# Optimization experiments

Hardware: AMD Instinct MI355X
Metric: run time of the kernel (lower is better)

The kernel has to match this reference:

```python
import jax, jax.numpy as jnp
import numpy as np

HIDDEN = 256
B, SQ, SKV = 8, 2048, 2048
SCALE = float(np.sqrt(HIDDEN / 2.0))  # module uses sqrt(hidden_dim/2)


def setup_inputs() -> dict:
    key = jax.random.key(0)
    ks = jax.random.split(key, 9)
    s = 1.0 / np.sqrt(HIDDEN)
    return {
        "query": jax.random.normal(ks[0], (B, SQ, HIDDEN), jnp.float32),
        "key": jax.random.normal(ks[1], (B, SKV, HIDDEN), jnp.float32),
        "value": jax.random.normal(ks[2], (B, SKV, HIDDEN), jnp.float32),
        "Wq": jax.random.uniform(ks[3], (HIDDEN, HIDDEN), jnp.float32, -s, s),
        "bq": jax.random.uniform(ks[4], (HIDDEN,), jnp.float32, -s, s),
        "Wk": jax.random.uniform(ks[5], (HIDDEN, HIDDEN), jnp.float32, -s, s),
        "bk": jax.random.uniform(ks[6], (HIDDEN,), jnp.float32, -s, s),
        "Wv": jax.random.uniform(ks[7], (HIDDEN, HIDDEN), jnp.float32, -s, s),
        "bv": jax.random.uniform(ks[8], (HIDDEN,), jnp.float32, -s, s),
    }


def reference(query, key, value, Wq, bq, Wk, bk, Wv, bv):
    # Linear projections (torch Linear: x @ W.T + b)
    Q = jnp.einsum('bsd,ed->bse', query, Wq) + bq  # [B,SQ,H]
    K = jnp.einsum('bsd,ed->bse', key, Wk) + bk    # [B,SKV,H]
    V = jnp.einsum('bsd,ed->bse', value, Wv) + bv  # [B,SKV,H]
    scores = jnp.einsum('bqd,bkd->bqk', Q, K) / SCALE  # [B,SQ,SKV]
    weights = jax.nn.softmax(scores, axis=-1)
    return jnp.einsum('bqk,bkd->bqd', weights, V)  # [B,SQ,H]
```

## Files before the change

kernel.cpp:

```cpp
#include <hip/hip_runtime.h>

#define HID 256
#define NB 8
#define SQL 2048
#define SKV 2048
#define SPLIT 4
#define KPB (SKV / SPLIT)
#define KVB 32
#define NT (KPB / KVB)
#define NROW (NB * SQL)

typedef __attribute__((ext_vector_type(8))) short bf16x8;
typedef __attribute__((ext_vector_type(4))) float f32x4;
typedef __attribute__((ext_vector_type(16))) float f32x16;

static __device__ __forceinline__ unsigned short f2bf(float x) {
  union { float f; unsigned int u; } v; v.f = x;
  unsigned int r = v.u + 0x7FFFu + ((v.u >> 16) & 1u);
  return (unsigned short)(r >> 16);
}

__global__ void wconv_kernel(const float* __restrict__ Wq, const float* __restrict__ Wk,
                             const float* __restrict__ Wv, unsigned short* __restrict__ out) {
  int i = blockIdx.x * blockDim.x + threadIdx.x;
  if (i >= 3 * HID * HID) return;
  const float* src = (i < HID * HID) ? Wq : (i < 2 * HID * HID ? Wk : Wv);
  out[i] = f2bf(src[i & (HID * HID - 1)]);
}

__global__ __launch_bounds__(512, 4) void proj_kernel(
    const float* __restrict__ query, const float* __restrict__ key, const float* __restrict__ value,
    const unsigned short* __restrict__ Wb,
    const float* __restrict__ bq, const float* __restrict__ bk, const float* __restrict__ bv,
    unsigned short* __restrict__ Qb, unsigned short* __restrict__ Kb, unsigned short* __restrict__ Vtb) {
  __shared__ __align__(16) char wl[65536];
  int tid = threadIdx.x;
  int wave = tid >> 6, lane = tid & 63, lr = lane & 15, lg = lane >> 4;
  int blk = blockIdx.x;
  int mat = blk >> 8;
  int rem = blk & 255;
  int b = rem >> 5;
  int rt = (rem >> 1) & 15;
  int et = rem & 1;

  const float* X = (mat == 0) ? query : (mat == 1 ? key : value);
  const float* bias = (mat == 0) ? bq : (mat == 1 ? bk : bv);
  const char* Wsrc = (const char*)(Wb + mat * HID * HID + et * 128 * HID);

#pragma unroll
  for (int i = 0; i < 8; i++) {
    int c = i * 512 + tid;
    int e = c >> 5;
    int glo = e * 512 + (((c & 31) ^ (e & 7)) << 4);
    __builtin_amdgcn_global_load_lds(
        (const __attribute__((address_space(1))) unsigned int*)(Wsrc + glo),
        (__attribute__((address_space(3))) unsigned int*)(wl + c * 16), 16, 0, 0);
  }

  int row_a = rt * 128 + wave * 16 + lr;
  const float* xrow = X + ((size_t)(b * SQL + row_a)) * HID;
  bf16x8 af[8];
#pragma unroll
  for (int s = 0; s < 8; s++) {
    const float4* p = (const float4*)(xrow + s * 32 + lg * 8);
    float4 x0 = p[0], x1 = p[1];
    bf16x8 a;
    a[0] = (short)f2bf(x0.x); a[1] = (short)f2bf(x0.y); a[2] = (short)f2bf(x0.z); a[3] = (short)f2bf(x0.w);
    a[4] = (short)f2bf(x1.x); a[5] = (short)f2bf(x1.y); a[6] = (short)f2bf(x1.z); a[7] = (short)f2bf(x1.w);
    af[s] = a;
  }
  __syncthreads();

  int row_c = rt * 128 + wave * 16 + lg * 4;
#pragma unroll
  for (int eo = 0; eo < 8; eo++) {
    f32x4 acc = (f32x4){0.f, 0.f, 0.f, 0.f};
    int eL = eo * 16 + lr;
#pragma unroll
    for (int sl = 0; sl < 8; sl++) {
      bf16x8 bfr = *(const bf16x8*)(wl + eL * 512 + (((sl * 4 + lg) ^ (eL & 7)) << 4));
      acc = __builtin_amdgcn_mfma_f32_16x16x32_bf16(af[sl], bfr, acc, 0, 0, 0);
    }
    int e = et * 128 + eo * 16 + lr;
    float bv_ = bias[e];
    if (mat < 2) {
      unsigned short* dst = (mat == 0 ? Qb : Kb) + (size_t)(b * SQL) * HID;
#pragma unroll
      for (int i = 0; i < 4; i++)
        dst[(size_t)(row_c + i) * HID + e] = f2bf(acc[i] + bv_);
    } else {
      ushort4 v;
      v.x = f2bf(acc[0] + bv_); v.y = f2bf(acc[1] + bv_);
      v.z = f2bf(acc[2] + bv_); v.w = f2bf(acc[3] + bv_);
      *(ushort4*)(Vtb + ((size_t)(b * HID + e)) * SKV + row_c) = v;
    }
  }
}

__global__ __launch_bounds__(256, 2) void attn_kernel(
    const unsigned short* __restrict__ Qb, const unsigned short* __restrict__ Kb,
    const unsigned short* __restrict__ Vtb, unsigned short* __restrict__ Op,
    float* __restrict__ Ml) {
  __shared__ __align__(16) char KA[16384];
  __shared__ __align__(16) char KB[16384];
  __shared__ __align__(16) char VA[16384];
  __shared__ __align__(16) char VB[16384];
  int tid = threadIdx.x;
  int wave = tid >> 6, lane = tid & 63, l31 = lane & 31, h = lane >> 5;
  int bid = (blockIdx.x & 7) * 64 + (blockIdx.x >> 3);
  int b = bid >> 6, s = (bid >> 4) & 3, qt = bid & 15;
  int qrow0 = qt * 128 + wave * 32;
  int k0 = s * KPB;

  const char* Kc0 = (const char*)(Kb + (size_t)b * SKV * HID) + (size_t)k0 * (HID * 2);
  const char* Vc0 = (const char*)(Vtb + (size_t)b * HID * SKV) + (size_t)k0 * 2;

  int offK[4], offV[4];
#pragma unroll
  for (int i = 0; i < 4; i++) {
    int g = i * 256 + tid;
    int ky = g >> 5, cs = g & 31;
    offK[i] = ky * 512 + ((cs ^ ky) << 4);
    int d = g >> 2, ccs = g & 3;
    int cc = ccs ^ ((d >> 3) & 3);
    offV[i] = d * (SKV * 2) + cc * 16;
  }

  auto stage = [&](int t, char* kdst, char* vdst) {
    const char* Ksrc = Kc0 + t * (KVB * HID * 2);
    const char* Vsrc = Vc0 + t * (KVB * 2);
#pragma unroll
    for (int i = 0; i < 4; i++)
      __builtin_amdgcn_global_load_lds(
          (const __attribute__((address_space(1))) unsigned int*)(Ksrc + offK[i]),
          (__attribute__((address_space(3))) unsigned int*)(kdst + (i * 256 + tid) * 16),
          16, 0, 0);
#pragma unroll
    for (int i = 0; i < 4; i++)
      __builtin_amdgcn_global_load_lds(
          (const __attribute__((address_space(1))) unsigned int*)(Vsrc + offV[i]),
          (__attribute__((address_space(3))) unsigned int*)(vdst + (i * 256 + tid) * 16),
          16, 0, 0);
  };

  bf16x8 qf[16];
  {
    const unsigned short* qrow = Qb + ((size_t)(b * SQL + qrow0 + l31)) * HID + h * 8;
#pragma unroll
    for (int ks = 0; ks < 16; ks++) qf[ks] = *(const bf16x8*)(qrow + ks * 16);
  }

  f32x16 acc[8];
#pragma unroll
  for (int dt = 0; dt < 8; dt++)
#pragma unroll
    for (int j = 0; j < 16; j++) acc[dt][j] = 0.f;

  float m = -1e30f, l = 0.f;
  const float kC = 1.44269504088896341f / 11.3137084989847604f;

  auto step = [&](const char* kb, const char* vb) {
    f32x16 p, p1;
#pragma unroll
    for (int j = 0; j < 16; j++) { p[j] = 0.f; p1[j] = 0.f; }
#pragma unroll
    for (int ks = 0; ks < 8; ks++) {
      bf16x8 kf0 = *(const bf16x8*)(kb + l31 * 512 + (((ks * 2 + h) ^ l31) << 4));
      bf16x8 kf1 = *(const bf16x8*)(kb + l31 * 512 + ((((ks + 8) * 2 + h) ^ l31) << 4));
      p = __builtin_amdgcn_mfma_f32_32x32x16_bf16(kf0, qf[ks], p, 0, 0, 0);
      p1 = __builtin_amdgcn_mfma_f32_32x32x16_bf16(kf1, qf[ks + 8], p1, 0, 0, 0);
    }
#pragma unroll
    for (int j = 0; j < 16; j++) p[j] += p1[j];

    float tmax = p[0];
#pragma unroll
    for (int j = 1; j < 16; j++) tmax = fmaxf(tmax, p[j]);
    tmax = fmaxf(tmax, __shfl_xor(tmax, 32, 64));
    float msc = tmax * kC;
    if (!__all(msc <= m + 8.0f)) {
      float mn = fmaxf(m, msc);
      float al = exp2f(m - mn);
      l *= al;
      m = mn;
#pragma unroll
      for (int r = 0; r < 16; r++) {
        int qp = (r & 3) + 8 * (r >> 2) + 4 * h;
        float ar = __shfl(al, qp, 64);
#pragma unroll
        for (int dt = 0; dt < 8; dt++) acc[dt][r] *= ar;
      }
    }
#pragma unroll
    for (int j = 0; j < 16; j++) p[j] = exp2f(fmaf(p[j], kC, -m));
    float ts = 0.f;
#pragma unroll
    for (int j = 0; j < 16; j++) ts += p[j];
    ts += __shfl_xor(ts, 32, 64);
    l += ts;

#pragma unroll
    for (int k2 = 0; k2 < 2; k2++) {
      unsigned P0, P1, P2, P3;
      asm("v_cvt_pk_bf16_f32 %0, %1, %2" : "=v"(P0) : "v"(p[k2 * 8 + 0]), "v"(p[k2 * 8 + 1]));
      asm("v_cvt_pk_bf16_f32 %0, %1, %2" : "=v"(P1) : "v"(p[k2 * 8 + 2]), "v"(p[k2 * 8 + 3]));
      asm("v_cvt_pk_bf16_f32 %0, %1, %2" : "=v"(P2) : "v"(p[k2 * 8 + 4]), "v"(p[k2 * 8 + 5]));
      asm("v_cvt_pk_bf16_f32 %0, %1, %2" : "=v"(P3) : "v"(p[k2 * 8 + 6]), "v"(p[k2 * 8 + 7]));
      asm("v_permlane32_swap_b32 %0, %1" : "+v"(P0), "+v"(P2));
      asm("v_permlane32_swap_b32 %0, %1" : "+v"(P1), "+v"(P3));
      union { unsigned u[4]; bf16x8 v; } pa;
      pa.u[0] = P0; pa.u[1] = P1; pa.u[2] = P2; pa.u[3] = P3;
      int ccs_base = k2 * 2 + h;
#pragma unroll
      for (int dt = 0; dt < 8; dt++) {
        int ccs = (ccs_base ^ ((l31 >> 3) & 3)) & 3;
        bf16x8 vf = *(const bf16x8*)(vb + dt * 2048 + l31 * 64 + ccs * 16);
        acc[dt] = __builtin_amdgcn_mfma_f32_32x32x16_bf16(pa.v, vf, acc[dt], 0, 0, 0);
      }
    }
  };

  stage(0, KA, VA);
  __syncthreads();
  for (int t = 0; t < NT; t++) {
    char* kb = (t & 1) ? KB : KA;
    char* vb = (t & 1) ? VB : VA;
    if (t + 1 < NT) stage(t + 1, (t & 1) ? KA : KB, (t & 1) ? VA : VB);
    step(kb, vb);
    __syncthreads();
  }

  if (h == 0) {
    size_t row = (size_t)b * SQL + qrow0 + l31;
    float2 ml; ml.x = m; ml.y = l;
    *(float2*)(Ml + ((size_t)s * NROW + row) * 2) = ml;
  }
#pragma unroll
  for (int r = 0; r < 16; r++) {
    int qp = (r & 3) + 8 * (r >> 2) + 4 * h;
    float linv = 1.0f / __shfl(l, qp, 64);
    size_t row = (size_t)b * SQL + qrow0 + qp;
#pragma unroll
    for (int dt = 0; dt < 8; dt++) {
      union { _Float16 hf; unsigned short u; } cv;
      cv.hf = (_Float16)(acc[dt][r] * linv);
      Op[((size_t)s * NROW + row) * HID + dt * 32 + l31] = cv.u;
    }
  }
}

__global__ __launch_bounds__(256) void comb_kernel(const unsigned short* __restrict__ Op,
                                                   const float* __restrict__ Ml,
                                                   float* __restrict__ out) {
  int idx = blockIdx.x * 256 + threadIdx.x;
  int row = idx >> 6;
  int d0 = (idx & 63) << 2;
  float mv[SPLIT], lv[SPLIT];
#pragma unroll
  for (int s = 0; s < SPLIT; s++) {
    float2 ml = *(const float2*)(Ml + ((size_t)s * NROW + row) * 2);
    mv[s] = ml.x; lv[s] = ml.y;
  }
  float M = mv[0];
#pragma unroll
  for (int s = 1; s < SPLIT; s++) M = fmaxf(M, mv[s]);
  float W = 0.f, w[SPLIT];
#pragma unroll
  for (int s = 0; s < SPLIT; s++) { w[s] = lv[s] * exp2f(mv[s] - M); W += w[s]; }
  float wi = 1.0f / W;
  float o0 = 0.f, o1 = 0.f, o2 = 0.f, o3 = 0.f;
#pragma unroll
  for (int s = 0; s < SPLIT; s++) {
    ushort4 u = *(const ushort4*)(Op + ((size_t)s * NROW + row) * HID + d0);
    union { unsigned short us; _Float16 hf; } c0, c1, c2, c3;
    c0.us = u.x; c1.us = u.y; c2.us = u.z; c3.us = u.w;
    o0 += w[s] * (float)c0.hf; o1 += w[s] * (float)c1.hf;
    o2 += w[s] * (float)c2.hf; o3 += w[s] * (float)c3.hf;
  }
  float4 res; res.x = o0 * wi; res.y = o1 * wi; res.z = o2 * wi; res.w = o3 * wi;
  *(float4*)(out + (size_t)row * HID + d0) = res;
}

extern "C" void kernel_launch(void* const* d_in, const int* in_sizes, int n_in,
                              void* d_out, int out_size, void* d_ws, size_t ws_size,
                              hipStream_t stream) {
  const float* query = (const float*)d_in[0];
  const float* key   = (const float*)d_in[1];
  const float* value = (const float*)d_in[2];
  const float* Wq = (const float*)d_in[3];
  const float* bq = (const float*)d_in[4];
  const float* Wk = (const float*)d_in[5];
  const float* bk = (const float*)d_in[6];
  const float* Wv = (const float*)d_in[7];
  const float* bv = (const float*)d_in[8];

  char* ws = (char*)d_ws;
  unsigned short* Wb  = (unsigned short*)ws;
  unsigned short* Qb  = (unsigned short*)(ws + 393216);
  unsigned short* Kb  = Qb + (size_t)NB * SQL * HID;
  unsigned short* Vtb = Kb + (size_t)NB * SKV * HID;
  unsigned short* Op  = Vtb + (size_t)NB * HID * SKV;
  float* Ml = (float*)(Op + (size_t)SPLIT * NROW * HID);

  hipLaunchKernelGGL(wconv_kernel, dim3(768), dim3(256), 0, stream, Wq, Wk, Wv, Wb);
  hipLaunchKernelGGL(proj_kernel, dim3(768), dim3(512), 0, stream,
                     query, key, value, Wb, bq, bk, bv, Qb, Kb, Vtb);
  hipLaunchKernelGGL(attn_kernel, dim3(512), dim3(256), 0, stream, Qb, Kb, Vtb, Op, Ml);
  hipLaunchKernelGGL(comb_kernel, dim3(4096), dim3(256), 0, stream, Op, Ml, (float*)d_out);
}
```

Measured before the change: 108.0 us.

## Rewrite attention to 16x16 MFMA tiles with direct global K/V loads

Reworks the attention kernel so each wave handles 16 query rows using 16x16x32 bf16 MFMAs instead of 32x32x16. K and V fragments are loaded straight from global memory into registers, replacing the double-buffered LDS staging; only a small per-wave LDS buffer remains to transpose P. The KV split drops from 4 to 2, which halves the partial outputs the combine kernel must merge. The cost is more redundant global/L2 traffic for K/V, since waves no longer share staged tiles, and less overlap between loads and compute.

```diff
diff --git a/kernel.cpp b/kernel.cpp
--- a/kernel.cpp
+++ b/kernel.cpp
@@ -4,7 +4,7 @@
 #define NB 8
 #define SQL 2048
 #define SKV 2048
-#define SPLIT 4
+#define SPLIT 2
 #define KPB (SKV / SPLIT)
 #define KVB 32
 #define NT (KPB / KVB)
@@ -12,7 +12,6 @@
 
 typedef __attribute__((ext_vector_type(8))) short bf16x8;
 typedef __attribute__((ext_vector_type(4))) float f32x4;
-typedef __attribute__((ext_vector_type(16))) float f32x16;
 
 static __device__ __forceinline__ unsigned short f2bf(float x) {
   union { float f; unsigned int u; } v; v.f = x;
@@ -101,150 +100,112 @@
     const unsigned short* __restrict__ Qb, const unsigned short* __restrict__ Kb,
     const unsigned short* __restrict__ Vtb, unsigned short* __restrict__ Op,
     float* __restrict__ Ml) {
-  __shared__ __align__(16) char KA[16384];
-  __shared__ __align__(16) char KB[16384];
-  __shared__ __align__(16) char VA[16384];
-  __shared__ __align__(16) char VB[16384];
+  __shared__ __align__(16) char PB[4][1024];
   int tid = threadIdx.x;
-  int wave = tid >> 6, lane = tid & 63, l31 = lane & 31, h = lane >> 5;
-  int bid = (blockIdx.x & 7) * 64 + (blockIdx.x >> 3);
-  int b = bid >> 6, s = (bid >> 4) & 3, qt = bid & 15;
-  int qrow0 = qt * 128 + wave * 32;
-  int k0 = s * KPB;
-
-  const char* Kc0 = (const char*)(Kb + (size_t)b * SKV * HID) + (size_t)k0 * (HID * 2);
-  const char* Vc0 = (const char*)(Vtb + (size_t)b * HID * SKV) + (size_t)k0 * 2;
-
-  int offK[4], offV[4];
-#pragma unroll
-  for (int i = 0; i < 4; i++) {
-    int g = i * 256 + tid;
-    int ky = g >> 5, cs = g & 31;
-    offK[i] = ky * 512 + ((cs ^ ky) << 4);
-    int d = g >> 2, ccs = g & 3;
-    int cc = ccs ^ ((d >> 3) & 3);
-    offV[i] = d * (SKV * 2) + cc * 16;
-  }
-
-  auto stage = [&](int t, char* kdst, char* vdst) {
-    const char* Ksrc = Kc0 + t * (KVB * HID * 2);
-    const char* Vsrc = Vc0 + t * (KVB * 2);
-#pragma unroll
-    for (int i = 0; i < 4; i++)
-      __builtin_amdgcn_global_load_lds(
-          (const __attribute__((address_space(1))) unsigned int*)(Ksrc + offK[i]),
-          (__attribute__((address_space(3))) unsigned int*)(kdst + (i * 256 + tid) * 16),
-          16, 0, 0);
-#pragma unroll
-    for (int i = 0; i < 4; i++)
-      __builtin_amdgcn_global_load_lds(
-          (const __attribute__((address_space(1))) unsigned int*)(Vsrc + offV[i]),
-          (__attribute__((address_space(3))) unsigned int*)(vdst + (i * 256 + tid) * 16),
-          16, 0, 0);
-  };
-
-  bf16x8 qf[16];
+  int wave = tid >> 6, lane = tid & 63, l15 = lane & 15, g = lane >> 4;
+  int j = blockIdx.x;
+  int p_ = (j & 7) + ((j >> 8) & 1) * 8;
+  int i_ = (j >> 3) & 31;
+  int b = p_ >> 1, s = p_ & 1;
+  int q0 = (i_ * 4 + wave) * 16;
+
+  const unsigned short* Kbase = Kb + ((size_t)b * SKV + (size_t)s * KPB) * HID;
+  const unsigned short* Vbase = Vtb + (size_t)b * HID * SKV + (size_t)s * KPB;
+
+  bf16x8 qf[8];
   {
-    const unsigned short* qrow = Qb + ((size_t)(b * SQL + qrow0 + l31)) * HID + h * 8;
-#pragma unroll
-    for (int ks = 0; ks < 16; ks++) qf[ks] = *(const bf16x8*)(qrow + ks * 16);
-  }
-
-  f32x16 acc[8];
-#pragma unroll
-  for (int dt = 0; dt < 8; dt++)
-#pragma unroll
-    for (int j = 0; j < 16; j++) acc[dt][j] = 0.f;
-
-  float m = -1e30f, l = 0.f;
+    const unsigned short* qrow = Qb + ((size_t)(b * SQL + q0 + l15)) * HID + g * 8;
+#pragma unroll
+    for (int sl = 0; sl < 8; sl++) qf[sl] = *(const bf16x8*)(qrow + sl * 32);
+  }
+
+  f32x4 acc[16];
+#pragma unroll
+  for (int dt = 0; dt < 16; dt++) acc[dt] = (f32x4){0.f, 0.f, 0.f, 0.f};
+  float m = -1e30f, lsum = 0.f;
   const float kC = 1.44269504088896341f / 11.3137084989847604f;
-
-  auto step = [&](const char* kb, const char* vb) {
-    f32x16 p, p1;
-#pragma unroll
-    for (int j = 0; j < 16; j++) { p[j] = 0.f; p1[j] = 0.f; }
-#pragma unroll
-    for (int ks = 0; ks < 8; ks++) {
-      bf16x8 kf0 = *(const bf16x8*)(kb + l31 * 512 + (((ks * 2 + h) ^ l31) << 4));
-      bf16x8 kf1 = *(const bf16x8*)(kb + l31 * 512 + ((((ks + 8) * 2 + h) ^ l31) << 4));
-      p = __builtin_amdgcn_mfma_f32_32x32x16_bf16(kf0, qf[ks], p, 0, 0, 0);
-      p1 = __builtin_amdgcn_mfma_f32_32x32x16_bf16(kf1, qf[ks + 8], p1, 0, 0, 0);
-    }
-#pragma unroll
-    for (int j = 0; j < 16; j++) p[j] += p1[j];
-
-    float tmax = p[0];
-#pragma unroll
-    for (int j = 1; j < 16; j++) tmax = fmaxf(tmax, p[j]);
+  char* pb = PB[wave];
+
+  for (int t = 0; t < NT; t++) {
+    __builtin_amdgcn_s_barrier();
+    int k0 = t * KVB;
+    const unsigned short* Kt = Kbase + (size_t)k0 * HID;
+
+    bf16x8 kf0[8], kf1[8];
+#pragma unroll
+    for (int sl = 0; sl < 8; sl++) {
+      kf0[sl] = *(const bf16x8*)(Kt + (size_t)l15 * HID + sl * 32 + g * 8);
+      kf1[sl] = *(const bf16x8*)(Kt + (size_t)(16 + l15) * HID + sl * 32 + g * 8);
+    }
+    f32x4 p0 = (f32x4){0.f, 0.f, 0.f, 0.f}, p1 = (f32x4){0.f, 0.f, 0.f, 0.f};
+#pragma unroll
+    for (int sl = 0; sl < 8; sl++) {
+      p0 = __builtin_amdgcn_mfma_f32_16x16x32_bf16(kf0[sl], qf[sl], p0, 0, 0, 0);
+      p1 = __builtin_amdgcn_mfma_f32_16x16x32_bf16(kf1[sl], qf[sl], p1, 0, 0, 0);
+    }
+
+    bf16x8 vf[16];
+#pragma unroll
+    for (int dt = 0; dt < 16; dt++)
+      vf[dt] = *(const bf16x8*)(Vbase + (size_t)(dt * 16 + l15) * SKV + k0 + g * 8);
+
+    float tmax = fmaxf(fmaxf(fmaxf(p0[0], p0[1]), fmaxf(p0[2], p0[3])),
+                       fmaxf(fmaxf(p1[0], p1[1]), fmaxf(p1[2], p1[3])));
+    tmax = fmaxf(tmax, __shfl_xor(tmax, 16, 64));
     tmax = fmaxf(tmax, __shfl_xor(tmax, 32, 64));
     float msc = tmax * kC;
     if (!__all(msc <= m + 8.0f)) {
       float mn = fmaxf(m, msc);
       float al = exp2f(m - mn);
-      l *= al;
+      lsum *= al;
       m = mn;
 #pragma unroll
-      for (int r = 0; r < 16; r++) {
-        int qp = (r & 3) + 8 * (r >> 2) + 4 * h;
-        float ar = __shfl(al, qp, 64);
-#pragma unroll
-        for (int dt = 0; dt < 8; dt++) acc[dt][r] *= ar;
+      for (int i = 0; i < 4; i++) {
+        float ar = __shfl(al, g * 4 + i, 64);
+#pragma unroll
+        for (int dt = 0; dt < 16; dt++) acc[dt][i] *= ar;
       }
     }
 #pragma unroll
-    for (int j = 0; j < 16; j++) p[j] = exp2f(fmaf(p[j], kC, -m));
-    float ts = 0.f;
-#pragma unroll
-    for (int j = 0; j < 16; j++) ts += p[j];
+    for (int i = 0; i < 4; i++) {
+      p0[i] = exp2f(fmaf(p0[i], kC, -m));
+      p1[i] = exp2f(fmaf(p1[i], kC, -m));
+    }
+    float ts = (p0[0] + p0[1]) + (p0[2] + p0[3]) + (p1[0] + p1[1]) + (p1[2] + p1[3]);
+    ts += __shfl_xor(ts, 16, 64);
     ts += __shfl_xor(ts, 32, 64);
-    l += ts;
-
-#pragma unroll
-    for (int k2 = 0; k2 < 2; k2++) {
-      unsigned P0, P1, P2, P3;
-      asm("v_cvt_pk_bf16_f32 %0, %1, %2" : "=v"(P0) : "v"(p[k2 * 8 + 0]), "v"(p[k2 * 8 + 1]));
-      asm("v_cvt_pk_bf16_f32 %0, %1, %2" : "=v"(P1) : "v"(p[k2 * 8 + 2]), "v"(p[k2 * 8 + 3]));
-      asm("v_cvt_pk_bf16_f32 %0, %1, %2" : "=v"(P2) : "v"(p[k2 * 8 + 4]), "v"(p[k2 * 8 + 5]));
-      asm("v_cvt_pk_bf16_f32 %0, %1, %2" : "=v"(P3) : "v"(p[k2 * 8 + 6]), "v"(p[k2 * 8 + 7]));
-      asm("v_permlane32_swap_b32 %0, %1" : "+v"(P0), "+v"(P2));
-      asm("v_permlane32_swap_b32 %0, %1" : "+v"(P1), "+v"(P3));
-      union { unsigned u[4]; bf16x8 v; } pa;
-      pa.u[0] = P0; pa.u[1] = P1; pa.u[2] = P2; pa.u[3] = P3;
-      int ccs_base = k2 * 2 + h;
-#pragma unroll
-      for (int dt = 0; dt < 8; dt++) {
-        int ccs = (ccs_base ^ ((l31 >> 3) & 3)) & 3;
-        bf16x8 vf = *(const bf16x8*)(vb + dt * 2048 + l31 * 64 + ccs * 16);
-        acc[dt] = __builtin_amdgcn_mfma_f32_32x32x16_bf16(pa.v, vf, acc[dt], 0, 0, 0);
-      }
-    }
-  };
-
-  stage(0, KA, VA);
-  __syncthreads();
-  for (int t = 0; t < NT; t++) {
-    char* kb = (t & 1) ? KB : KA;
-    char* vb = (t & 1) ? VB : VA;
-    if (t + 1 < NT) stage(t + 1, (t & 1) ? KA : KB, (t & 1) ? VA : VB);
-    step(kb, vb);
-    __syncthreads();
-  }
-
-  if (h == 0) {
-    size_t row = (size_t)b * SQL + qrow0 + l31;
-    float2 ml; ml.x = m; ml.y = l;
-    *(float2*)(Ml + ((size_t)s * NROW + row) * 2) = ml;
-  }
-#pragma unroll
-  for (int r = 0; r < 16; r++) {
-    int qp = (r & 3) + 8 * (r >> 2) + 4 * h;
-    float linv = 1.0f / __shfl(l, qp, 64);
-    size_t row = (size_t)b * SQL + qrow0 + qp;
-#pragma unroll
-    for (int dt = 0; dt < 8; dt++) {
+    lsum += ts;
+
+    unsigned u0, u1, u2, u3;
+    asm("v_cvt_pk_bf16_f32 %0, %1, %2" : "=v"(u0) : "v"(p0[0]), "v"(p0[1]));
+    asm("v_cvt_pk_bf16_f32 %0, %1, %2" : "=v"(u1) : "v"(p0[2]), "v"(p0[3]));
+    asm("v_cvt_pk_bf16_f32 %0, %1, %2" : "=v"(u2) : "v"(p1[0]), "v"(p1[1]));
+    asm("v_cvt_pk_bf16_f32 %0, %1, %2" : "=v"(u3) : "v"(p1[2]), "v"(p1[3]));
+    uint2 w0; w0.x = u0; w0.y = u1;
+    uint2 w1; w1.x = u2; w1.y = u3;
+    *(uint2*)(pb + l15 * 64 + g * 8) = w0;
+    *(uint2*)(pb + l15 * 64 + 32 + g * 8) = w1;
+    bf16x8 pa = *(const bf16x8*)(pb + l15 * 64 + g * 16);
+
+#pragma unroll
+    for (int dt = 0; dt < 16; dt++)
+      acc[dt] = __builtin_amdgcn_mfma_f32_16x16x32_bf16(pa, vf[dt], acc[dt], 0, 0, 0);
+  }
+
+  if (g == 0) {
+    float2 ml; ml.x = m; ml.y = lsum;
+    *(float2*)(Ml + ((size_t)s * NROW + (size_t)b * SQL + q0 + l15) * 2) = ml;
+  }
+#pragma unroll
+  for (int i = 0; i < 4; i++) {
+    int q = g * 4 + i;
+    float linv = 1.0f / __shfl(lsum, q, 64);
+    size_t row = (size_t)b * SQL + q0 + q;
+#pragma unroll
+    for (int dt = 0; dt < 16; dt++) {
       union { _Float16 hf; unsigned short u; } cv;
-      cv.hf = (_Float16)(acc[dt][r] * linv);
-      Op[((size_t)s * NROW + row) * HID + dt * 32 + l31] = cv.u;
+      cv.hf = (_Float16)(acc[dt][i] * linv);
+      Op[((size_t)s * NROW + row) * HID + dt * 16 + l15] = cv.u;
     }
   }
 }
```

After: 271.0 us. 151% more time.

## Enlarge attention blocks to 8 waves with 64-key tiles and finer waits

Applied to the files above, without the earlier changes.

The attention kernel now runs 512 threads per block. Each block covers 256 query rows and loads 64-key K/V tiles into a 128 KB dynamic shared-memory double buffer, so each staged tile is reused by twice as many waves. The per-iteration __syncthreads is replaced by explicit vmcnt waits and raw barriers, so the next tile's prefetch can stay in flight while the current tile is computed. The trade-offs are one block per CU with no overlap between blocks, a single dependent MFMA chain per substep instead of two interleaved accumulators, and reliance on the launch accepting 128 KB of dynamic LDS.

```diff
diff --git a/kernel.cpp b/kernel.cpp
--- a/kernel.cpp
+++ b/kernel.cpp
@@ -6,7 +6,7 @@
 #define SKV 2048
 #define SPLIT 4
 #define KPB (SKV / SPLIT)
-#define KVB 32
+#define KVB 64
 #define NT (KPB / KVB)
 #define NROW (NB * SQL)
 
@@ -97,57 +97,46 @@
   }
 }
 
-__global__ __launch_bounds__(256, 2) void attn_kernel(
+__global__ __launch_bounds__(512, 2) void attn_kernel(
     const unsigned short* __restrict__ Qb, const unsigned short* __restrict__ Kb,
     const unsigned short* __restrict__ Vtb, unsigned short* __restrict__ Op,
     float* __restrict__ Ml) {
-  __shared__ __align__(16) char KA[16384];
-  __shared__ __align__(16) char KB[16384];
-  __shared__ __align__(16) char VA[16384];
-  __shared__ __align__(16) char VB[16384];
+  extern __shared__ char smem[];
   int tid = threadIdx.x;
   int wave = tid >> 6, lane = tid & 63, l31 = lane & 31, h = lane >> 5;
-  int bid = (blockIdx.x & 7) * 64 + (blockIdx.x >> 3);
-  int b = bid >> 6, s = (bid >> 4) & 3, qt = bid & 15;
-  int qrow0 = qt * 128 + wave * 32;
-  int k0 = s * KPB;
-
-  const char* Kc0 = (const char*)(Kb + (size_t)b * SKV * HID) + (size_t)k0 * (HID * 2);
-  const char* Vc0 = (const char*)(Vtb + (size_t)b * HID * SKV) + (size_t)k0 * 2;
-
-  int offK[4], offV[4];
-#pragma unroll
-  for (int i = 0; i < 4; i++) {
-    int g = i * 256 + tid;
-    int ky = g >> 5, cs = g & 31;
-    offK[i] = ky * 512 + ((cs ^ ky) << 4);
-    int d = g >> 2, ccs = g & 3;
-    int cc = ccs ^ ((d >> 3) & 3);
-    offV[i] = d * (SKV * 2) + cc * 16;
-  }
-
-  auto stage = [&](int t, char* kdst, char* vdst) {
-    const char* Ksrc = Kc0 + t * (KVB * HID * 2);
-    const char* Vsrc = Vc0 + t * (KVB * 2);
-#pragma unroll
-    for (int i = 0; i < 4; i++)
+  int L = (blockIdx.x & 7) * 32 + (blockIdx.x >> 3);
+  int b = L >> 5, sp = (L >> 3) & 3, qt = L & 7;
+  int q0 = qt * 256 + wave * 32;
+
+  const char* Kc0 = (const char*)Kb + ((size_t)b * SKV + (size_t)sp * KPB) * (HID * 2);
+  const char* Vc0 = (const char*)Vtb + (size_t)b * HID * SKV * 2 + (size_t)sp * KPB * 2;
+
+  auto stage = [&](int t, char* kb, char* vb) {
+    const char* Ks = Kc0 + t * (KVB * HID * 2);
+    const char* Vs = Vc0 + t * (KVB * 2);
+#pragma unroll
+    for (int i = 0; i < 4; i++) {
+      int g = i * 512 + tid;
+      int ky = g >> 5, cs = g & 31;
       __builtin_amdgcn_global_load_lds(
-          (const __attribute__((address_space(1))) unsigned int*)(Ksrc + offK[i]),
-          (__attribute__((address_space(3))) unsigned int*)(kdst + (i * 256 + tid) * 16),
-          16, 0, 0);
-#pragma unroll
-    for (int i = 0; i < 4; i++)
+          (const __attribute__((address_space(1))) unsigned int*)(Ks + ky * 512 + ((cs ^ (ky & 31)) << 4)),
+          (__attribute__((address_space(3))) unsigned int*)(kb + g * 16), 16, 0, 0);
+    }
+#pragma unroll
+    for (int i = 0; i < 4; i++) {
+      int g = i * 512 + tid;
+      int d = g >> 3, cs = g & 7;
       __builtin_amdgcn_global_load_lds(
-          (const __attribute__((address_space(1))) unsigned int*)(Vsrc + offV[i]),
-          (__attribute__((address_space(3))) unsigned int*)(vdst + (i * 256 + tid) * 16),
-          16, 0, 0);
+          (const __attribute__((address_space(1))) unsigned int*)(Vs + (size_t)d * (SKV * 2) + ((cs ^ (d & 7)) << 4)),
+          (__attribute__((address_space(3))) unsigned int*)(vb + g * 16), 16, 0, 0);
+    }
   };
 
   bf16x8 qf[16];
   {
-    const unsigned short* qrow = Qb + ((size_t)(b * SQL + qrow0 + l31)) * HID + h * 8;
-#pragma unroll
-    for (int ks = 0; ks < 16; ks++) qf[ks] = *(const bf16x8*)(qrow + ks * 16);
+    const unsigned short* qrow = Qb + ((size_t)(b * SQL + q0 + l31)) * HID + h * 8;
+#pragma unroll
+    for (int s = 0; s < 16; s++) qf[s] = *(const bf16x8*)(qrow + s * 16);
   }
 
   f32x16 acc[8];
@@ -156,22 +145,18 @@
 #pragma unroll
     for (int j = 0; j < 16; j++) acc[dt][j] = 0.f;
 
-  float m = -1e30f, l = 0.f;
+  float m = -1e30f, lsum = 0.f;
   const float kC = 1.44269504088896341f / 11.3137084989847604f;
 
-  auto step = [&](const char* kb, const char* vb) {
-    f32x16 p, p1;
-#pragma unroll
-    for (int j = 0; j < 16; j++) { p[j] = 0.f; p1[j] = 0.f; }
-#pragma unroll
-    for (int ks = 0; ks < 8; ks++) {
-      bf16x8 kf0 = *(const bf16x8*)(kb + l31 * 512 + (((ks * 2 + h) ^ l31) << 4));
-      bf16x8 kf1 = *(const bf16x8*)(kb + l31 * 512 + ((((ks + 8) * 2 + h) ^ l31) << 4));
-      p = __builtin_amdgcn_mfma_f32_32x32x16_bf16(kf0, qf[ks], p, 0, 0, 0);
-      p1 = __builtin_amdgcn_mfma_f32_32x32x16_bf16(kf1, qf[ks + 8], p1, 0, 0, 0);
-    }
-#pragma unroll
-    for (int j = 0; j < 16; j++) p[j] += p1[j];
+  auto substep = [&](const char* kb, const char* vb, int kt) {
+    f32x16 p;
+#pragma unroll
+    for (int j = 0; j < 16; j++) p[j] = 0.f;
+#pragma unroll
+    for (int s = 0; s < 16; s++) {
+      bf16x8 kf = *(const bf16x8*)(kb + (kt * 32 + l31) * 512 + (((2 * s + h) ^ l31) << 4));
+      p = __builtin_amdgcn_mfma_f32_32x32x16_bf16(kf, qf[s], p, 0, 0, 0);
+    }
 
     float tmax = p[0];
 #pragma unroll
@@ -181,7 +166,7 @@
     if (!__all(msc <= m + 8.0f)) {
       float mn = fmaxf(m, msc);
       float al = exp2f(m - mn);
-      l *= al;
+      lsum *= al;
       m = mn;
 #pragma unroll
       for (int r = 0; r < 16; r++) {
@@ -197,7 +182,7 @@
 #pragma unroll
     for (int j = 0; j < 16; j++) ts += p[j];
     ts += __shfl_xor(ts, 32, 64);
-    l += ts;
+    lsum += ts;
 
 #pragma unroll
     for (int k2 = 0; k2 < 2; k2++) {
@@ -210,41 +195,46 @@
       asm("v_permlane32_swap_b32 %0, %1" : "+v"(P1), "+v"(P3));
       union { unsigned u[4]; bf16x8 v; } pa;
       pa.u[0] = P0; pa.u[1] = P1; pa.u[2] = P2; pa.u[3] = P3;
-      int ccs_base = k2 * 2 + h;
+      int c = kt * 4 + k2 * 2 + h;
 #pragma unroll
       for (int dt = 0; dt < 8; dt++) {
-        int ccs = (ccs_base ^ ((l31 >> 3) & 3)) & 3;
-        bf16x8 vf = *(const bf16x8*)(vb + dt * 2048 + l31 * 64 + ccs * 16);
+        bf16x8 vf = *(const bf16x8*)(vb + (dt * 32 + l31) * 128 + (((c ^ (l31 & 7)) & 7) << 4));
         acc[dt] = __builtin_amdgcn_mfma_f32_32x32x16_bf16(pa.v, vf, acc[dt], 0, 0, 0);
       }
     }
   };
 
-  stage(0, KA, VA);
-  __syncthreads();
+  stage(0, smem, smem + 65536);
   for (int t = 0; t < NT; t++) {
-    char* kb = (t & 1) ? KB : KA;
-    char* vb = (t & 1) ? VB : VA;
-    if (t + 1 < NT) stage(t + 1, (t & 1) ? KA : KB, (t & 1) ? VA : VB);
-    step(kb, vb);
-    __syncthreads();
+    const char* kb = smem + (t & 1) * 32768;
+    const char* vb = smem + 65536 + (t & 1) * 32768;
+    if (t + 1 < NT) {
+      stage(t + 1, smem + ((t + 1) & 1) * 32768, smem + 65536 + ((t + 1) & 1) * 32768);
+      asm volatile("s_waitcnt vmcnt(8)" ::: "memory");
+    } else {
+      asm volatile("s_waitcnt vmcnt(0)" ::: "memory");
+    }
+    __builtin_amdgcn_s_barrier();
+    __builtin_amdgcn_sched_barrier(0);
+    substep(kb, vb, 0);
+    substep(kb, vb, 1);
+    __builtin_amdgcn_s_barrier();
   }
 
   if (h == 0) {
-    size_t row = (size_t)b * SQL + qrow0 + l31;
-    float2 ml; ml.x = m; ml.y = l;
-    *(float2*)(Ml + ((size_t)s * NROW + row) * 2) = ml;
+    float2 ml; ml.x = m; ml.y = lsum;
+    *(float2*)(Ml + ((size_t)sp * NROW + (size_t)b * SQL + q0 + l31) * 2) = ml;
   }
 #pragma unroll
   for (int r = 0; r < 16; r++) {
     int qp = (r & 3) + 8 * (r >> 2) + 4 * h;
-    float linv = 1.0f / __shfl(l, qp, 64);
-    size_t row = (size_t)b * SQL + qrow0 + qp;
+    float linv = 1.0f / __shfl(lsum, qp, 64);
+    size_t row = (size_t)b * SQL + q0 + qp;
 #pragma unroll
     for (int dt = 0; dt < 8; dt++) {
       union { _Float16 hf; unsigned short u; } cv;
       cv.hf = (_Float16)(acc[dt][r] * linv);
-      Op[((size_t)s * NROW + row) * HID + dt * 32 + l31] = cv.u;
+      Op[((size_t)sp * NROW + row) * HID + dt * 32 + l31] = cv.u;
     }
   }
 }
@@ -305,6 +295,6 @@
   hipLaunchKernelGGL(wconv_kernel, dim3(768), dim3(256), 0, stream, Wq, Wk, Wv, Wb);
   hipLaunchKernelGGL(proj_kernel, dim3(768), dim3(512), 0, stream,
                      query, key, value, Wb, bq, bk, bv, Qb, Kb, Vtb);
-  hipLaunchKernelGGL(attn_kernel, dim3(512), dim3(256), 0, stream, Qb, Kb, Vtb, Op, Ml);
+  hipLaunchKernelGGL(attn_kernel, dim3(256), dim3(512), 131072, stream, Qb, Kb, Vtb, Op, Ml);
   hipLaunchKernelGGL(comb_kernel, dim3(4096), dim3(256), 0, stream, Op, Ml, (float*)d_out);
 }
```

New measurement: 103.1 us. 4.5% less time.
